# Kernel tuning notes

Measured on AMD Instinct MI355X. Metric: run time of the kernel, lower is better.

Reference implementation:

```python
import jax, jax.numpy as jnp
import numpy as np

H, W = 512, 512
ROWS_PER_CHUNK = 32  # H must be divisible; 16 chunks
TWO_PI = 2.0 * np.pi
ALPHA_MIN = 1.0 / 255.0  # rasterizer skip threshold
ALPHA_MAX = 0.999        # rasterizer alpha clamp


def setup_inputs() -> dict:
    key = jax.random.key(0)
    k0, k1, k2, k3 = jax.random.split(key, 4)
    N = 2048
    xyz = jax.random.uniform(k0, (N, 2), jnp.float32, -1.0, 1.0)      # NDC means
    scaling = jax.random.uniform(k1, (N, 2), jnp.float32, 2.0, 12.0)  # pixel-space stds
    rotation = jax.random.normal(k2, (N, 1), jnp.float32)             # pre-sigmoid angle
    features = jax.random.uniform(k3, (N, 3), jnp.float32)            # RGB
    opacity = jnp.ones((N, 1), jnp.float32)
    return {"xyz": xyz, "scaling": scaling, "rotation": rotation,
            "features": features, "opacity": opacity}


def reference(xyz, scaling, rotation, features, opacity):
    # --- project_gaussians_2d_scale_rot ---
    theta = jax.nn.sigmoid(rotation[:, 0]) * TWO_PI          # get_rotation
    s = jnp.abs(scaling)                                      # get_scaling
    cos, sin = jnp.cos(theta), jnp.sin(theta)
    s0, s1 = s[:, 0] ** 2, s[:, 1] ** 2
    # cov = R diag(s^2) R^T  -> [[a,b],[b,c]]
    a = cos * cos * s0 + sin * sin * s1
    b = cos * sin * (s0 - s1)
    c = sin * sin * s0 + cos * cos * s1
    inv_det = 1.0 / (a * c - b * b)
    c0, c1, c2 = c * inv_det, -b * inv_det, a * inv_det       # conic = cov^-1
    # NDC [-1,1] -> pixel centers (gsplat ndc2pix)
    xys = 0.5 * ((xyz + 1.0) * jnp.array([W, H], jnp.float32) - 1.0)  # [N,2]
    op = opacity[:, 0]

    xs = jnp.arange(W, dtype=jnp.float32)
    ys = jnp.arange(H, dtype=jnp.float32)
    dx = xs[:, None] - xys[None, :, 0]                        # [W,N]
    dx2_half_c0 = 0.5 * c0 * dx * dx                          # [W,N], reused per row block

    def render_rows(yb):
        # yb: [R] row y-coordinates
        dy = yb[:, None, None] - xys[None, None, :, 1]        # [R,1,N]
        sigma = dx2_half_c0[None] + 0.5 * c2 * dy * dy + c1 * dx[None] * dy  # [R,W,N]
        alpha = jnp.minimum(ALPHA_MAX, op * jnp.exp(-sigma))
        alpha = jnp.where(alpha < ALPHA_MIN, 0.0, alpha)
        return jnp.einsum('rwn,nc->rwc', alpha, features)     # [R,W,3]

    out = jax.lax.map(render_rows, ys.reshape(-1, ROWS_PER_CHUNK))  # [C,R,W,3]
    out = jnp.clip(out.reshape(H, W, 3), 0.0, 1.0)
    return out.transpose(2, 0, 1)[None]                       # [1,3,H,W]
```

## Files before the change

kernel.cpp:

```cpp
#include <hip/hip_runtime.h>
#include <math.h>

#define W_IMG 512
#define H_IMG 512
#define ALPHA_MIN (1.0f/255.0f)
#define ALPHA_MAX 0.999f
#define NMAX_CHUNK 256

__global__ __launch_bounds__(256) void precompute_params(
    const float* __restrict__ xyz,
    const float* __restrict__ scaling,
    const float* __restrict__ rotation,
    const float* __restrict__ features,
    const float* __restrict__ opacity,
    float4* __restrict__ G0, float4* __restrict__ G1, float4* __restrict__ G2,
    int N)
{
  const int i = blockIdx.x * 256 + threadIdx.x;
  if (i >= N) return;
  const float rx = rotation[i];
  const float theta = 6.28318530717958647692f / (1.0f + __expf(-rx));
  float sn, cs;
  __sincosf(theta, &sn, &cs);
  const float sxa = fabsf(scaling[2*i+0]);
  const float sya = fabsf(scaling[2*i+1]);
  const float s0 = sxa*sxa, s1 = sya*sya;
  const float a = cs*cs*s0 + sn*sn*s1;
  const float b = cs*sn*(s0 - s1);
  const float c = sn*sn*s0 + cs*cs*s1;
  const float inv_det = 1.0f / (a*c - b*b);
  const float h0 = 0.5f * c * inv_det;
  const float h1 = -b * inv_det;
  const float h2 = 0.5f * a * inv_det;
  const float mx = 0.5f*((xyz[2*i+0] + 1.0f)*(float)W_IMG - 1.0f);
  const float my = 0.5f*((xyz[2*i+1] + 1.0f)*(float)H_IMG - 1.0f);
  const float op = opacity[i];
  float r2 = -1.0f;
  if (op > 0.0f) {
    const float T = __logf(255.0f * op);
    if (T > 0.0f) r2 = 2.0f * T * fmaxf(s0, s1) * 1.0001f + 1e-2f;
  }
  G0[i] = make_float4(mx, my, h0, h1);
  G1[i] = make_float4(h2, r2, op, 0.0f);
  G2[i] = make_float4(features[3*i+0], features[3*i+1], features[3*i+2], 0.0f);
}

__global__ __launch_bounds__(256) void splat_render(
    const float4* __restrict__ G0,
    const float4* __restrict__ G1,
    const float4* __restrict__ G2,
    float* __restrict__ out, int N)
{
  __shared__ float4 sA[NMAX_CHUNK];
  __shared__ float4 sB[NMAX_CHUNK];
  __shared__ float  sOp[NMAX_CHUNK];
  __shared__ int wcnt[4];

  const int tid = threadIdx.x;
  const int tile_x = blockIdx.x << 4;
  const int tile_y = blockIdx.y << 4;
  const int lx = tid & 15, ly = tid >> 4;
  const float px = (float)(tile_x + lx);
  const float py = (float)(tile_y + ly);
  const float tx0 = (float)tile_x, tx1 = (float)(tile_x + 15);
  const float ty0 = (float)tile_y, ty1 = (float)(tile_y + 15);

  float acc0 = 0.f, acc1 = 0.f, acc2 = 0.f;

  for (int base = 0; base < N; base += NMAX_CHUNK) {
    const int gi = base + tid;
    bool keep = false;
    float4 g0 = make_float4(0,0,0,0), g1 = make_float4(0,0,0,0), g2 = make_float4(0,0,0,0);
    if (gi < N) {
      g0 = G0[gi]; g1 = G1[gi]; g2 = G2[gi];
      const float ddx = fmaxf(fmaxf(tx0 - g0.x, g0.x - tx1), 0.0f);
      const float ddy = fmaxf(fmaxf(ty0 - g0.y, g0.y - ty1), 0.0f);
      keep = (ddx*ddx + ddy*ddy) <= g1.y;
    }
    const unsigned long long m = __ballot(keep);
    const int lane = tid & 63, wid = tid >> 6;
    const int pre = __popcll(m & ((1ull << lane) - 1ull));
    if (lane == 0) wcnt[wid] = __popcll(m);
    __syncthreads();
    int wbase = 0, total = 0;
    #pragma unroll
    for (int w = 0; w < 4; ++w) { const int cw = wcnt[w]; if (w < wid) wbase += cw; total += cw; }
    if (keep) {
      const int p = wbase + pre;
      sA[p] = make_float4(g0.x, g0.y, g0.z, g0.w);
      sB[p] = make_float4(g1.x, g2.x, g2.y, g2.z);
      sOp[p] = g1.z;
    }
    __syncthreads();
    for (int j = 0; j < total; ++j) {
      const float4 gA = sA[j];
      const float4 gB = sB[j];
      const float opj = sOp[j];
      const float dx = px - gA.x;
      const float dy = py - gA.y;
      const float sig = fmaf(dx, fmaf(gA.z, dx, gA.w*dy), gB.x*dy*dy);
      const float e = __expf(-sig);
      float alpha = fminf(ALPHA_MAX, opj * e);
      alpha = (alpha < ALPHA_MIN) ? 0.0f : alpha;
      acc0 = fmaf(alpha, gB.y, acc0);
      acc1 = fmaf(alpha, gB.z, acc1);
      acc2 = fmaf(alpha, gB.w, acc2);
    }
    __syncthreads();
  }

  const int x = tile_x + lx, y = tile_y + ly;
  const int pix = y * W_IMG + x;
  out[pix]                 = fminf(fmaxf(acc0, 0.0f), 1.0f);
  out[W_IMG*H_IMG + pix]   = fminf(fmaxf(acc1, 0.0f), 1.0f);
  out[2*W_IMG*H_IMG + pix] = fminf(fmaxf(acc2, 0.0f), 1.0f);
}

extern "C" void kernel_launch(void* const* d_in, const int* in_sizes, int n_in,
                              void* d_out, int out_size, void* d_ws, size_t ws_size,
                              hipStream_t stream) {
  const float* xyz      = (const float*)d_in[0];
  const float* scaling  = (const float*)d_in[1];
  const float* rotation = (const float*)d_in[2];
  const float* features = (const float*)d_in[3];
  const float* opacity  = (const float*)d_in[4];
  float* out = (float*)d_out;
  const int N = in_sizes[0] / 2;

  char* ws = (char*)d_ws;
  float4* G0 = (float4*)(ws);
  float4* G1 = (float4*)(ws + 16*2048);
  float4* G2 = (float4*)(ws + 32*2048);

  precompute_params<<<(N + 255)/256, 256, 0, stream>>>(
      xyz, scaling, rotation, features, opacity, G0, G1, G2, N);
  dim3 grid(W_IMG / 16, H_IMG / 16);
  splat_render<<<grid, 256, 0, stream>>>(G0, G1, G2, out, N);
}
```

Baseline: 73.67 us.

## Fuse Gaussian projection into render kernel and tighten tile culling bounds

Removes the separate precompute kernel, so each render block recomputes conic, center and cull radius for every Gaussian directly from the raw inputs. This drops one kernel launch and the workspace round trip. The per-tile cull test gains axis-aligned extent checks based on the covariance diagonals, so fewer Gaussians pass into the inner loop. Features are loaded only for Gaussians that survive culling. In exchange, every one of the 1024 blocks redoes the transcendental parameter math for all Gaussians.

```diff
diff --git a/kernel.cpp b/kernel.cpp
--- a/kernel.cpp
+++ b/kernel.cpp
@@ -5,55 +5,19 @@
 #define H_IMG 512
 #define ALPHA_MIN (1.0f/255.0f)
 #define ALPHA_MAX 0.999f
-#define NMAX_CHUNK 256
+#define CHUNK 256
 
-__global__ __launch_bounds__(256) void precompute_params(
+__global__ __launch_bounds__(256) void splat_fused(
     const float* __restrict__ xyz,
     const float* __restrict__ scaling,
     const float* __restrict__ rotation,
     const float* __restrict__ features,
     const float* __restrict__ opacity,
-    float4* __restrict__ G0, float4* __restrict__ G1, float4* __restrict__ G2,
-    int N)
-{
-  const int i = blockIdx.x * 256 + threadIdx.x;
-  if (i >= N) return;
-  const float rx = rotation[i];
-  const float theta = 6.28318530717958647692f / (1.0f + __expf(-rx));
-  float sn, cs;
-  __sincosf(theta, &sn, &cs);
-  const float sxa = fabsf(scaling[2*i+0]);
-  const float sya = fabsf(scaling[2*i+1]);
-  const float s0 = sxa*sxa, s1 = sya*sya;
-  const float a = cs*cs*s0 + sn*sn*s1;
-  const float b = cs*sn*(s0 - s1);
-  const float c = sn*sn*s0 + cs*cs*s1;
-  const float inv_det = 1.0f / (a*c - b*b);
-  const float h0 = 0.5f * c * inv_det;
-  const float h1 = -b * inv_det;
-  const float h2 = 0.5f * a * inv_det;
-  const float mx = 0.5f*((xyz[2*i+0] + 1.0f)*(float)W_IMG - 1.0f);
-  const float my = 0.5f*((xyz[2*i+1] + 1.0f)*(float)H_IMG - 1.0f);
-  const float op = opacity[i];
-  float r2 = -1.0f;
-  if (op > 0.0f) {
-    const float T = __logf(255.0f * op);
-    if (T > 0.0f) r2 = 2.0f * T * fmaxf(s0, s1) * 1.0001f + 1e-2f;
-  }
-  G0[i] = make_float4(mx, my, h0, h1);
-  G1[i] = make_float4(h2, r2, op, 0.0f);
-  G2[i] = make_float4(features[3*i+0], features[3*i+1], features[3*i+2], 0.0f);
-}
-
-__global__ __launch_bounds__(256) void splat_render(
-    const float4* __restrict__ G0,
-    const float4* __restrict__ G1,
-    const float4* __restrict__ G2,
     float* __restrict__ out, int N)
 {
-  __shared__ float4 sA[NMAX_CHUNK];
-  __shared__ float4 sB[NMAX_CHUNK];
-  __shared__ float  sOp[NMAX_CHUNK];
+  __shared__ float4 sA[CHUNK];
+  __shared__ float4 sB[CHUNK];
+  __shared__ float  sOp[CHUNK];
   __shared__ int wcnt[4];
 
   const int tid = threadIdx.x;
@@ -67,16 +31,50 @@
 
   float acc0 = 0.f, acc1 = 0.f, acc2 = 0.f;
 
-  for (int base = 0; base < N; base += NMAX_CHUNK) {
+  for (int base = 0; base < N; base += CHUNK) {
     const int gi = base + tid;
     bool keep = false;
-    float4 g0 = make_float4(0,0,0,0), g1 = make_float4(0,0,0,0), g2 = make_float4(0,0,0,0);
+    float mx = 0.f, my = 0.f, h0 = 0.f, h1 = 0.f, h2 = 0.f, op = 0.f;
+    float f0 = 0.f, f1 = 0.f, f2 = 0.f;
     if (gi < N) {
-      g0 = G0[gi]; g1 = G1[gi]; g2 = G2[gi];
-      const float ddx = fmaxf(fmaxf(tx0 - g0.x, g0.x - tx1), 0.0f);
-      const float ddy = fmaxf(fmaxf(ty0 - g0.y, g0.y - ty1), 0.0f);
-      keep = (ddx*ddx + ddy*ddy) <= g1.y;
+      const float2 xy = ((const float2*)xyz)[gi];
+      const float2 sc = ((const float2*)scaling)[gi];
+      const float rot = rotation[gi];
+      op = opacity[gi];
+      const float theta = 6.28318530717958647692f / (1.0f + __expf(-rot));
+      float sn, cs;
+      __sincosf(theta, &sn, &cs);
+      const float sxa = fabsf(sc.x), sya = fabsf(sc.y);
+      const float s0 = sxa*sxa, s1 = sya*sya;
+      const float a = cs*cs*s0 + sn*sn*s1;
+      const float b = cs*sn*(s0 - s1);
+      const float c = sn*sn*s0 + cs*cs*s1;
+      const float inv_det = 1.0f / (a*c - b*b);
+      h0 = 0.5f * c * inv_det;
+      h1 = -b * inv_det;
+      h2 = 0.5f * a * inv_det;
+      mx = 0.5f*((xy.x + 1.0f)*(float)W_IMG - 1.0f);
+      my = 0.5f*((xy.y + 1.0f)*(float)H_IMG - 1.0f);
+      if (op > 0.0f) {
+        const float T = __logf(255.0f * op);
+        if (T > 0.0f) {
+          const float T2 = 2.0f * T * 1.0005f;
+          const float rx2 = fmaf(T2, a, 0.05f);
+          const float ry2 = fmaf(T2, c, 0.05f);
+          const float rc2 = fmaf(T2, fmaxf(s0, s1), 0.05f);
+          const float ddx = fmaxf(fmaxf(tx0 - mx, mx - tx1), 0.0f);
+          const float ddy = fmaxf(fmaxf(ty0 - my, my - ty1), 0.0f);
+          const float dx2 = ddx*ddx, dy2 = ddy*ddy;
+          keep = (dx2 <= rx2) && (dy2 <= ry2) && (dx2 + dy2 <= rc2);
+        }
+      }
+      if (keep) {
+        f0 = features[3*gi+0];
+        f1 = features[3*gi+1];
+        f2 = features[3*gi+2];
+      }
     }
+
     const unsigned long long m = __ballot(keep);
     const int lane = tid & 63, wid = tid >> 6;
     const int pre = __popcll(m & ((1ull << lane) - 1ull));
@@ -87,11 +85,12 @@
     for (int w = 0; w < 4; ++w) { const int cw = wcnt[w]; if (w < wid) wbase += cw; total += cw; }
     if (keep) {
       const int p = wbase + pre;
-      sA[p] = make_float4(g0.x, g0.y, g0.z, g0.w);
-      sB[p] = make_float4(g1.x, g2.x, g2.y, g2.z);
-      sOp[p] = g1.z;
+      sA[p] = make_float4(mx, my, h0, h1);
+      sB[p] = make_float4(h2, f0, f1, f2);
+      sOp[p] = op;
     }
     __syncthreads();
+
     for (int j = 0; j < total; ++j) {
       const float4 gA = sA[j];
       const float4 gB = sB[j];
@@ -127,13 +126,9 @@
   float* out = (float*)d_out;
   const int N = in_sizes[0] / 2;
 
-  char* ws = (char*)d_ws;
-  float4* G0 = (float4*)(ws);
-  float4* G1 = (float4*)(ws + 16*2048);
-  float4* G2 = (float4*)(ws + 32*2048);
+  (void)d_ws; (void)ws_size;
 
-  precompute_params<<<(N + 255)/256, 256, 0, stream>>>(
-      xyz, scaling, rotation, features, opacity, G0, G1, G2, N);
   dim3 grid(W_IMG / 16, H_IMG / 16);
-  splat_render<<<grid, 256, 0, stream>>>(G0, G1, G2, out, N);
+  splat_fused<<<grid, 256, 0, stream>>>(xyz, scaling, rotation, features,
+                                        opacity, out, N);
 }
```

After: 74.80 us. About the same (+1.5%).
